# Performance work log

Hardware: AMD Instinct MI355X
Metric: run time of the kernel (lower is better)

The kernel has to match this reference:

```python
import jax, jax.numpy as jnp
import numpy as np

EMBED_DIM = 512
NUM_HEADS = 8
HEAD_DIM = EMBED_DIM // NUM_HEADS


def setup_inputs() -> dict:
    key = jax.random.key(0)
    k1, k2, k3, k4, k5, k6 = jax.random.split(key, 6)
    B, S, D = 2, 4096, EMBED_DIM
    scale = 1.0 / np.sqrt(D)
    return {
        "inputs": jax.random.normal(k1, (B, S, D), dtype=jnp.float32),
        "Wq": jax.random.normal(k2, (D, D), dtype=jnp.float32) * scale,
        "Wk": jax.random.normal(k3, (D, D), dtype=jnp.float32) * scale,
        "Wv": jax.random.normal(k4, (D, D), dtype=jnp.float32) * scale,
        "Wc": jax.random.normal(k5, (D, D), dtype=jnp.float32) * scale,
        "bc": jax.random.normal(k6, (D,), dtype=jnp.float32) * 0.01,
    }


def reference(inputs, Wq, Wk, Wv, Wc, bc):
    B, S, D = inputs.shape
    H, Hd = NUM_HEADS, HEAD_DIM

    def split_heads(x):
        # [B,S,D] -> [B,H,S,Hd]
        return x.reshape(B, S, H, Hd).transpose(0, 2, 1, 3)

    # nn.Linear applies x @ W.T
    q = split_heads(inputs @ Wq.T).astype(jnp.float32)
    k = split_heads(inputs @ Wk.T).astype(jnp.float32)
    v = split_heads(inputs @ Wv.T).astype(jnp.float32)

    scores = jnp.einsum("bhqd,bhkd->bhqk", q, k) / np.sqrt(Hd).astype(jnp.float32)
    weights = jax.nn.softmax(scores, axis=-1)
    attended = jnp.einsum("bhqk,bhkd->bhqd", weights, v).astype(inputs.dtype)
    attended = attended.transpose(0, 2, 1, 3).reshape(B, S, D)
    return attended @ Wc.T + bc
```

## Files before the change

kernel.cpp:

```cpp
#include <hip/hip_runtime.h>
#include <cstdint>
#include <cstddef>

typedef _Float16 half_t;
typedef half_t h8 __attribute__((ext_vector_type(8)));
typedef half_t h4 __attribute__((ext_vector_type(4)));
typedef float f4 __attribute__((ext_vector_type(4)));
typedef float f16v __attribute__((ext_vector_type(16)));
typedef unsigned int u32;

static constexpr int S_LEN  = 4096;
static constexpr int DMODEL = 512;
static constexpr int NH     = 8;
static constexpr int HD     = 64;
static constexpr int BATCH  = 2;
static constexpr int MTOK   = BATCH * S_LEN;

#define QSCALE 0.18033688011112043f

__device__ __forceinline__ void g2lds16(const void* g, void* l) {
    __builtin_amdgcn_global_load_lds(
        (const __attribute__((address_space(1))) u32*)(uintptr_t)g,
        (__attribute__((address_space(3))) u32*)(u32)(uintptr_t)l,
        16, 0, 0);
}

__device__ __forceinline__ f4 mfma16(h8 a, h8 b, f4 c) {
    return __builtin_amdgcn_mfma_f32_16x16x32_f16(a, b, c, 0, 0, 0);
}

__device__ __forceinline__ f16v mfma32(h8 a, h8 b, f16v c) {
    return __builtin_amdgcn_mfma_f32_32x32x16_f16(a, b, c, 0, 0, 0);
}

__device__ __forceinline__ u32 pkrtz(float a, float b) {
#if __has_builtin(__builtin_amdgcn_cvt_pkrtz)
    auto r = __builtin_amdgcn_cvt_pkrtz(a, b);
    return __builtin_bit_cast(u32, r);
#else
    union { half_t h[2]; u32 u; } x;
    x.h[0] = (half_t)a; x.h[1] = (half_t)b;
    return x.u;
#endif
}

__device__ __forceinline__ void plswap(u32 a, u32 b, u32& lo, u32& hi_, int hi) {
#if __has_builtin(__builtin_amdgcn_permlane32_swap)
    auto r = __builtin_amdgcn_permlane32_swap(a, b, false, false);
    lo = (u32)r[0]; hi_ = (u32)r[1];
#else
    u32 ta = __shfl_xor(a, 32);
    u32 tb = __shfl_xor(b, 32);
    lo  = hi ? tb : a;
    hi_ = hi ? b  : ta;
#endif
}

__global__ void cvt_all(const float* __restrict__ X,
                        const float* __restrict__ w0, const float* __restrict__ w1,
                        const float* __restrict__ w2, const float* __restrict__ w3,
                        half_t* __restrict__ Xh,
                        half_t* __restrict__ o0, half_t* __restrict__ o1,
                        half_t* __restrict__ o2, half_t* __restrict__ o3) {
    int bx = blockIdx.x;
    const float* in;
    half_t* out;
    float s = 1.0f;
    int i;
    if (bx < 2048) {
        in = X; out = Xh;
        i = (bx * 256 + threadIdx.x) * 8;
    } else {
        int y = (bx - 2048) >> 7;
        in  = (y==0) ? w0 : (y==1) ? w1 : (y==2) ? w2 : w3;
        out = (y==0) ? o0 : (y==1) ? o1 : (y==2) ? o2 : o3;
        if (y == 0) s = QSCALE;
        i = (((bx - 2048) & 127) * 256 + threadIdx.x) * 8;
    }
    const float4* p = (const float4*)(in + i);
    float4 a = p[0], b = p[1];
    h8 h;
    h[0]=(half_t)(a.x*s); h[1]=(half_t)(a.y*s); h[2]=(half_t)(a.z*s); h[3]=(half_t)(a.w*s);
    h[4]=(half_t)(b.x*s); h[5]=(half_t)(b.y*s); h[6]=(half_t)(b.z*s); h[7]=(half_t)(b.w*s);
    *(h8*)(out + i) = h;
}

__device__ __forceinline__ void gemm_core2(const half_t* __restrict__ A,
                                           const half_t* __restrict__ B,
                                           int m0, int n0, int Kdim,
                                           half_t* As, half_t* Bs,
                                           f4 (&acc)[2][4]) {
    const int tid  = threadIdx.x;
    const int lane = tid & 63;
    const int w    = tid >> 6;
    const int quad = lane >> 4;
    const int low  = lane & 15;
    const int wr   = (w >> 1) * 32;
    const int wc   = (w & 1) * 64;

    f4 zero = {0.f, 0.f, 0.f, 0.f};
    #pragma unroll
    for (int i = 0; i < 2; ++i)
        #pragma unroll
        for (int j = 0; j < 4; ++j) acc[i][j] = zero;

    auto stage = [&](int kk, int p) {
        {
            int c = tid;
            int row = c >> 2, cs = c & 3;
            int gc = cs ^ ((row >> 1) & 3);
            g2lds16(A + (size_t)(m0 + row) * Kdim + kk + gc * 8, As + p * 2048 + c * 8);
        }
        #pragma unroll
        for (int it = 0; it < 2; ++it) {
            int c = tid + 256 * it;
            int row = c >> 2, cs = c & 3;
            int gc = cs ^ ((row >> 1) & 3);
            g2lds16(B + (size_t)(n0 + row) * Kdim + kk + gc * 8, Bs + p * 4096 + c * 8);
        }
    };

    stage(0, 0);
    const int T = Kdim / 32;
    for (int t = 0; t < T; ++t) {
        __syncthreads();
        if (t + 1 < T) stage((t + 1) * 32, (t + 1) & 1);

        const half_t* Ac = As + (t & 1) * 2048;
        const half_t* Bc = Bs + (t & 1) * 4096;
        h8 af[2], bf[4];
        #pragma unroll
        for (int i = 0; i < 2; ++i) {
            int r = wr + i * 16 + low;
            af[i] = *(const h8*)(Ac + r * 32 + (quad ^ ((r >> 1) & 3)) * 8);
        }
        #pragma unroll
        for (int j = 0; j < 4; ++j) {
            int r = wc + j * 16 + low;
            bf[j] = *(const h8*)(Bc + r * 32 + (quad ^ ((r >> 1) & 3)) * 8);
        }
        #pragma unroll
        for (int i = 0; i < 2; ++i)
            #pragma unroll
            for (int j = 0; j < 4; ++j)
                acc[i][j] = mfma16(af[i], bf[j], acc[i][j]);
    }
}

__global__ __launch_bounds__(256, 4) void gemm_proj(
    const half_t* __restrict__ X,
    const half_t* __restrict__ Wq, const half_t* __restrict__ Wk, const half_t* __restrict__ Wv,
    half_t* __restrict__ Q, half_t* __restrict__ K, half_t* __restrict__ Vt) {
    __shared__ half_t As[2 * 64 * 32];
    __shared__ half_t Bs[2 * 128 * 32];
    const int z  = blockIdx.z;
    const int bx = blockIdx.x;

    const half_t *A, *B;
    int m0, n0;
    if (z < 2) {
        A = X; B = (z == 0) ? Wq : Wk;
        m0 = (bx >> 2) * 64; n0 = (bx & 3) * 128;
    } else {
        A = Wv; B = X;
        m0 = (bx & 7) * 64; n0 = (bx >> 3) * 128;
    }
    f4 acc[2][4];
    gemm_core2(A, B, m0, n0, DMODEL, As, Bs, acc);

    const int lane = threadIdx.x & 63;
    const int w    = threadIdx.x >> 6;
    const int quad = lane >> 4, low = lane & 15;
    const int wr = (w >> 1) * 32, wc = (w & 1) * 64;

    if (z < 2) {
        half_t* O = (z == 0) ? Q : K;
        #pragma unroll
        for (int i = 0; i < 2; ++i) {
            int mb = m0 + wr + i * 16 + quad * 4;
            #pragma unroll
            for (int j = 0; j < 4; ++j) {
                int n = n0 + wc + j * 16 + low;
                int h = n >> 6, d = n & 63;
                #pragma unroll
                for (int r = 0; r < 4; ++r) {
                    int m = mb + r;
                    int b = m >> 12, s = m & 4095;
                    size_t idx = (((size_t)(b * NH + h) << 12) + s) * 64 + d;
                    O[idx] = (half_t)acc[i][j][r];
                }
            }
        }
    } else {
        #pragma unroll
        for (int i = 0; i < 2; ++i) {
            int dgb = m0 + wr + i * 16 + quad * 4;
            #pragma unroll
            for (int j = 0; j < 4; ++j) {
                int tok = n0 + wc + j * 16 + low;
                int b = tok >> 12, s = tok & 4095;
                #pragma unroll
                for (int r = 0; r < 4; ++r) {
                    int dg = dgb + r;
                    size_t idx = (((size_t)(b * NH + (dg >> 6)) << 18)) + ((dg & 63) << 12) + s;
                    Vt[idx] = (half_t)acc[i][j][r];
                }
            }
        }
    }
}

__global__ __launch_bounds__(256, 4) void gemm_out(
    const half_t* __restrict__ A, const half_t* __restrict__ W,
    const float* __restrict__ bias, float* __restrict__ out) {
    __shared__ half_t As[2 * 64 * 32];
    __shared__ half_t Bs[2 * 128 * 32];
    const int bx = blockIdx.x;
    const int m0 = (bx >> 2) * 64;
    const int n0 = (bx & 3) * 128;
    f4 acc[2][4];
    gemm_core2(A, W, m0, n0, DMODEL, As, Bs, acc);

    const int lane = threadIdx.x & 63;
    const int w    = threadIdx.x >> 6;
    const int quad = lane >> 4, low = lane & 15;
    const int wr = (w >> 1) * 32, wc = (w & 1) * 64;

    #pragma unroll
    for (int i = 0; i < 2; ++i) {
        int mb = m0 + wr + i * 16 + quad * 4;
        #pragma unroll
        for (int j = 0; j < 4; ++j) {
            int n = n0 + wc + j * 16 + low;
            float bv = bias[n];
            #pragma unroll
            for (int r = 0; r < 4; ++r)
                out[(size_t)(mb + r) * DMODEL + n] = acc[i][j][r] + bv;
        }
    }
}

__global__ __launch_bounds__(256, 2) void flash_attn(
    const half_t* __restrict__ Q,
    const half_t* __restrict__ K,
    const half_t* __restrict__ V,
    half_t* __restrict__ Oa) {
    __shared__ half_t Ks[2][128 * 64];
    __shared__ half_t Vs[2][64 * 128];

    const int tid  = threadIdx.x;
    const int lane = tid & 63;
    const int w    = tid >> 6;
    const int l31  = lane & 31;
    const int hi   = lane >> 5;
    const int bh   = blockIdx.y;
    const int q0   = blockIdx.x * 128 + w * 32;

    const half_t* Qb = Q + ((size_t)bh << 18);
    const half_t* Kb = K + ((size_t)bh << 18);
    const half_t* Vb = V + ((size_t)bh << 18);

    h8 qf[4];
    #pragma unroll
    for (int ks = 0; ks < 4; ++ks)
        qf[ks] = *(const h8*)(Qb + (size_t)(q0 + l31) * 64 + ks * 16 + hi * 8);

    f16v zz;
    #pragma unroll
    for (int r = 0; r < 16; ++r) zz[r] = 0.f;

    f16v Oacc[2];
    Oacc[0] = zz; Oacc[1] = zz;
    f4 rs = {0.f, 0.f, 0.f, 0.f};

    auto stage = [&](int k0, int p) {
        #pragma unroll
        for (int it = 0; it < 4; ++it) {
            int c = tid + 256 * it;
            int key = c >> 3, cs = c & 7;
            int gc = cs ^ (key & 7);
            g2lds16(Kb + (size_t)(k0 + key) * 64 + gc * 8, &Ks[p][c * 8]);
        }
        #pragma unroll
        for (int it = 0; it < 4; ++it) {
            int c = tid + 256 * it;
            int d = c >> 4, cs = c & 15;
            int gc = cs ^ (d & 7);
            g2lds16(Vb + (size_t)d * S_LEN + k0 + gc * 8, &Vs[p][c * 8]);
        }
    };

    stage(0, 0);

    for (int c = 0; c < S_LEN / 128; ++c) {
        __syncthreads();
        if (c + 1 < S_LEN / 128) stage((c + 1) * 128, (c + 1) & 1);

        const half_t* Kc = Ks[c & 1];
        const half_t* Vc = Vs[c & 1];

        f16v sc[4];
        #pragma unroll
        for (int nt = 0; nt < 4; ++nt) {
            int key = nt * 32 + l31;
            #pragma unroll
            for (int ks = 0; ks < 4; ++ks) {
                h8 kf = *(const h8*)(Kc + key * 64 + ((ks * 2 + hi) ^ (key & 7)) * 8);
                sc[nt] = mfma32(kf, qf[ks], ks == 0 ? zz : sc[nt]);
            }
        }

        #pragma unroll
        for (int nt = 0; nt < 4; ++nt) {
            float p[16];
            #pragma unroll
            for (int r = 0; r < 16; ++r) {
                p[r] = __builtin_amdgcn_exp2f(sc[nt][r]);
                rs[r & 3] += p[r];
            }
            u32 a0 = pkrtz(p[0],  p[1]);
            u32 a1 = pkrtz(p[2],  p[3]);
            u32 a2 = pkrtz(p[4],  p[5]);
            u32 a3 = pkrtz(p[6],  p[7]);
            u32 a4 = pkrtz(p[8],  p[9]);
            u32 a5 = pkrtz(p[10], p[11]);
            u32 a6 = pkrtz(p[12], p[13]);
            u32 a7 = pkrtz(p[14], p[15]);

            union H8U { u32 u[4]; h8 v; } b0, b1;
            plswap(a0, a2, b0.u[0], b0.u[2], hi);
            plswap(a1, a3, b0.u[1], b0.u[3], hi);
            plswap(a4, a6, b1.u[0], b1.u[2], hi);
            plswap(a5, a7, b1.u[1], b1.u[3], hi);

            #pragma unroll
            for (int dt = 0; dt < 2; ++dt) {
                int d = dt * 32 + l31;
                h8 vf0 = *(const h8*)(Vc + d * 128 + ((nt * 4 + 0 + hi) ^ (d & 7)) * 8);
                h8 vf1 = *(const h8*)(Vc + d * 128 + ((nt * 4 + 2 + hi) ^ (d & 7)) * 8);
                Oacc[dt] = mfma32(vf0, b0.v, Oacc[dt]);
                Oacc[dt] = mfma32(vf1, b1.v, Oacc[dt]);
            }
        }
    }

    float lsum = (rs[0] + rs[1]) + (rs[2] + rs[3]);
    lsum += __shfl_xor(lsum, 32);
    float inv = 1.0f / lsum;

    const int b = bh >> 3, h = bh & 7;
    half_t* Ob = Oa + ((size_t)(b * S_LEN + q0 + l31)) * DMODEL + h * 64;
    #pragma unroll
    for (int dt = 0; dt < 2; ++dt)
        #pragma unroll
        for (int rg = 0; rg < 4; ++rg) {
            h4 o;
            #pragma unroll
            for (int e = 0; e < 4; ++e) o[e] = (half_t)(Oacc[dt][rg * 4 + e] * inv);
            *(h4*)(Ob + dt * 32 + rg * 8 + hi * 4) = o;
        }
}

extern "C" void kernel_launch(void* const* d_in, const int* in_sizes, int n_in,
                              void* d_out, int out_size, void* d_ws, size_t ws_size,
                              hipStream_t stream) {
    const float* X  = (const float*)d_in[0];
    const float* Wq = (const float*)d_in[1];
    const float* Wk = (const float*)d_in[2];
    const float* Wv = (const float*)d_in[3];
    const float* Wc = (const float*)d_in[4];
    const float* bc = (const float*)d_in[5];
    float* out = (float*)d_out;

    char* ws = (char*)d_ws;
    const size_t SZ_X = (size_t)MTOK * DMODEL * 2;
    const size_t SZ_W = (size_t)DMODEL * DMODEL * 2;
    half_t* Xh   = (half_t*)(ws);
    half_t* Wqh  = (half_t*)(ws + SZ_X);
    half_t* Wkh  = (half_t*)(ws + SZ_X + SZ_W);
    half_t* Wvh  = (half_t*)(ws + SZ_X + 2 * SZ_W);
    half_t* Wch  = (half_t*)(ws + SZ_X + 3 * SZ_W);
    half_t* Qh   = (half_t*)(ws + SZ_X + 4 * SZ_W);
    half_t* Kh   = (half_t*)(ws + 2 * SZ_X + 4 * SZ_W);
    half_t* Vt   = (half_t*)(ws + 3 * SZ_X + 4 * SZ_W);
    half_t* Att  = (half_t*)(ws + 4 * SZ_X + 4 * SZ_W);

    cvt_all<<<2048 + 512, 256, 0, stream>>>(X, Wq, Wk, Wv, Wc, Xh, Wqh, Wkh, Wvh, Wch);
    gemm_proj<<<dim3(512, 1, 3), 256, 0, stream>>>(Xh, Wqh, Wkh, Wvh, Qh, Kh, Vt);
    flash_attn<<<dim3(32, 16), 256, 0, stream>>>(Qh, Kh, Vt, Att);
    gemm_out<<<512, 256, 0, stream>>>(Att, Wch, bc, out);
}
```

Before: 203.8 us.

## Store MFMA fragments contiguously in LDS and double GEMM K-tile to 64

The GEMM and attention kernels now write global data into LDS already arranged in MFMA-fragment order, so each lane reads its operand with a single contiguous lane*8 offset. This replaces the XOR swizzle and per-fragment address arithmetic. The GEMM K step grows from 32 to 64, halving the number of barrier iterations, at the cost of twice the shared memory and a lower occupancy hint (4 to 3 blocks). Global loads become less contiguous per row (16-byte chunks scattered across rows), which may cost memory coalescing efficiency.

```diff
diff --git a/kernel.cpp b/kernel.cpp
--- a/kernel.cpp
+++ b/kernel.cpp
@@ -85,7 +85,7 @@
     *(h8*)(out + i) = h;
 }
 
-__device__ __forceinline__ void gemm_core2(const half_t* __restrict__ A,
+__device__ __forceinline__ void gemm_core3(const half_t* __restrict__ A,
                                            const half_t* __restrict__ B,
                                            int m0, int n0, int Kdim,
                                            half_t* As, half_t* Bs,
@@ -93,10 +93,8 @@
     const int tid  = threadIdx.x;
     const int lane = tid & 63;
     const int w    = tid >> 6;
+    const int low  = lane & 15;
     const int quad = lane >> 4;
-    const int low  = lane & 15;
-    const int wr   = (w >> 1) * 32;
-    const int wc   = (w & 1) * 64;
 
     f4 zero = {0.f, 0.f, 0.f, 0.f};
     #pragma unroll
@@ -104,55 +102,60 @@
         #pragma unroll
         for (int j = 0; j < 4; ++j) acc[i][j] = zero;
 
-    auto stage = [&](int kk, int p) {
-        {
-            int c = tid;
-            int row = c >> 2, cs = c & 3;
-            int gc = cs ^ ((row >> 1) & 3);
-            g2lds16(A + (size_t)(m0 + row) * Kdim + kk + gc * 8, As + p * 2048 + c * 8);
-        }
+    auto stage = [&](int kk0, int p) {
         #pragma unroll
         for (int it = 0; it < 2; ++it) {
             int c = tid + 256 * it;
-            int row = c >> 2, cs = c & 3;
-            int gc = cs ^ ((row >> 1) & 3);
-            g2lds16(B + (size_t)(n0 + row) * Kdim + kk + gc * 8, Bs + p * 4096 + c * 8);
+            int row = m0 + (c >> 7) * 16 + low;
+            int col = kk0 + ((c >> 6) & 1) * 32 + quad * 8;
+            g2lds16(A + (size_t)row * Kdim + col, As + p * 4096 + c * 8);
+        }
+        #pragma unroll
+        for (int it = 0; it < 4; ++it) {
+            int c = tid + 256 * it;
+            int row = n0 + (c >> 7) * 16 + low;
+            int col = kk0 + ((c >> 6) & 1) * 32 + quad * 8;
+            g2lds16(B + (size_t)row * Kdim + col, Bs + p * 8192 + c * 8);
         }
     };
 
     stage(0, 0);
-    const int T = Kdim / 32;
+    const int T = Kdim / 64;
+    const int aoff = (w >> 1) * 2048 + lane * 8;
+    const int boff = (w & 1) * 4096 + lane * 8;
     for (int t = 0; t < T; ++t) {
         __syncthreads();
-        if (t + 1 < T) stage((t + 1) * 32, (t + 1) & 1);
-
-        const half_t* Ac = As + (t & 1) * 2048;
-        const half_t* Bc = Bs + (t & 1) * 4096;
-        h8 af[2], bf[4];
-        #pragma unroll
-        for (int i = 0; i < 2; ++i) {
-            int r = wr + i * 16 + low;
-            af[i] = *(const h8*)(Ac + r * 32 + (quad ^ ((r >> 1) & 3)) * 8);
-        }
-        #pragma unroll
-        for (int j = 0; j < 4; ++j) {
-            int r = wc + j * 16 + low;
-            bf[j] = *(const h8*)(Bc + r * 32 + (quad ^ ((r >> 1) & 3)) * 8);
-        }
+        if (t + 1 < T) stage((t + 1) * 64, (t + 1) & 1);
+
+        const half_t* Al = As + (t & 1) * 4096 + aoff;
+        const half_t* Bl = Bs + (t & 1) * 8192 + boff;
+        h8 af[2][2], bf[4][2];
         #pragma unroll
         for (int i = 0; i < 2; ++i)
             #pragma unroll
-            for (int j = 0; j < 4; ++j)
-                acc[i][j] = mfma16(af[i], bf[j], acc[i][j]);
-    }
-}
-
-__global__ __launch_bounds__(256, 4) void gemm_proj(
+            for (int kk = 0; kk < 2; ++kk)
+                af[i][kk] = *(const h8*)(Al + i * 1024 + kk * 512);
+        #pragma unroll
+        for (int j = 0; j < 4; ++j)
+            #pragma unroll
+            for (int kk = 0; kk < 2; ++kk)
+                bf[j][kk] = *(const h8*)(Bl + j * 1024 + kk * 512);
+        #pragma unroll
+        for (int kk = 0; kk < 2; ++kk)
+            #pragma unroll
+            for (int i = 0; i < 2; ++i)
+                #pragma unroll
+                for (int j = 0; j < 4; ++j)
+                    acc[i][j] = mfma16(af[i][kk], bf[j][kk], acc[i][j]);
+    }
+}
+
+__global__ __launch_bounds__(256, 3) void gemm_proj(
     const half_t* __restrict__ X,
     const half_t* __restrict__ Wq, const half_t* __restrict__ Wk, const half_t* __restrict__ Wv,
     half_t* __restrict__ Q, half_t* __restrict__ K, half_t* __restrict__ Vt) {
-    __shared__ half_t As[2 * 64 * 32];
-    __shared__ half_t Bs[2 * 128 * 32];
+    __shared__ half_t As[2 * 64 * 64];
+    __shared__ half_t Bs[2 * 128 * 64];
     const int z  = blockIdx.z;
     const int bx = blockIdx.x;
 
@@ -166,7 +169,7 @@
         m0 = (bx & 7) * 64; n0 = (bx >> 3) * 128;
     }
     f4 acc[2][4];
-    gemm_core2(A, B, m0, n0, DMODEL, As, Bs, acc);
+    gemm_core3(A, B, m0, n0, DMODEL, As, Bs, acc);
 
     const int lane = threadIdx.x & 63;
     const int w    = threadIdx.x >> 6;
@@ -210,16 +213,16 @@
     }
 }
 
-__global__ __launch_bounds__(256, 4) void gemm_out(
+__global__ __launch_bounds__(256, 3) void gemm_out(
     const half_t* __restrict__ A, const half_t* __restrict__ W,
     const float* __restrict__ bias, float* __restrict__ out) {
-    __shared__ half_t As[2 * 64 * 32];
-    __shared__ half_t Bs[2 * 128 * 32];
+    __shared__ half_t As[2 * 64 * 64];
+    __shared__ half_t Bs[2 * 128 * 64];
     const int bx = blockIdx.x;
     const int m0 = (bx >> 2) * 64;
     const int n0 = (bx & 3) * 128;
     f4 acc[2][4];
-    gemm_core2(A, W, m0, n0, DMODEL, As, Bs, acc);
+    gemm_core3(A, W, m0, n0, DMODEL, As, Bs, acc);
 
     const int lane = threadIdx.x & 63;
     const int w    = threadIdx.x >> 6;
@@ -277,16 +280,16 @@
         #pragma unroll
         for (int it = 0; it < 4; ++it) {
             int c = tid + 256 * it;
-            int key = c >> 3, cs = c & 7;
-            int gc = cs ^ (key & 7);
-            g2lds16(Kb + (size_t)(k0 + key) * 64 + gc * 8, &Ks[p][c * 8]);
+            int key = k0 + (c >> 8) * 32 + l31;
+            int col = ((c >> 6) & 3) * 16 + hi * 8;
+            g2lds16(Kb + (size_t)key * 64 + col, &Ks[p][c * 8]);
         }
         #pragma unroll
         for (int it = 0; it < 4; ++it) {
             int c = tid + 256 * it;
-            int d = c >> 4, cs = c & 15;
-            int gc = cs ^ (d & 7);
-            g2lds16(Vb + (size_t)d * S_LEN + k0 + gc * 8, &Vs[p][c * 8]);
+            int d   = (c >> 9) * 32 + l31;
+            int key = k0 + ((c >> 6) & 7) * 16 + hi * 8;
+            g2lds16(Vb + (size_t)d * S_LEN + key, &Vs[p][c * 8]);
         }
     };
 
@@ -296,16 +299,15 @@
         __syncthreads();
         if (c + 1 < S_LEN / 128) stage((c + 1) * 128, (c + 1) & 1);
 
-        const half_t* Kc = Ks[c & 1];
-        const half_t* Vc = Vs[c & 1];
+        const half_t* Kl = Ks[c & 1] + lane * 8;
+        const half_t* Vl = Vs[c & 1] + lane * 8;
 
         f16v sc[4];
         #pragma unroll
         for (int nt = 0; nt < 4; ++nt) {
-            int key = nt * 32 + l31;
             #pragma unroll
             for (int ks = 0; ks < 4; ++ks) {
-                h8 kf = *(const h8*)(Kc + key * 64 + ((ks * 2 + hi) ^ (key & 7)) * 8);
+                h8 kf = *(const h8*)(Kl + nt * 2048 + ks * 512);
                 sc[nt] = mfma32(kf, qf[ks], ks == 0 ? zz : sc[nt]);
             }
         }
@@ -335,9 +337,8 @@
 
             #pragma unroll
             for (int dt = 0; dt < 2; ++dt) {
-                int d = dt * 32 + l31;
-                h8 vf0 = *(const h8*)(Vc + d * 128 + ((nt * 4 + 0 + hi) ^ (d & 7)) * 8);
-                h8 vf1 = *(const h8*)(Vc + d * 128 + ((nt * 4 + 2 + hi) ^ (d & 7)) * 8);
+                h8 vf0 = *(const h8*)(Vl + dt * 4096 + (nt * 2 + 0) * 512);
+                h8 vf1 = *(const h8*)(Vl + dt * 4096 + (nt * 2 + 1) * 512);
                 Oacc[dt] = mfma32(vf0, b0.v, Oacc[dt]);
                 Oacc[dt] = mfma32(vf1, b1.v, Oacc[dt]);
             }
```

After: 216.0 us. 6.0% more time.

## Enlarge GEMM tiles to 128x128 and pre-fragment K/V LDS layout in attention

Applied to the files above, without the earlier changes.

The projection and output GEMMs move from 64x128 to 128x128 block tiles, with each wave computing 64x64 and accumulating in a 4x4 MFMA grid. This halves the grid and raises data reuse per LDS load, at the cost of more registers and LDS per block and lower occupancy (launch bounds 3). The flash attention kernel now stages K and V into LDS already arranged in MFMA fragment order, so each lane reads contiguous 16-byte chunks at a fixed offset instead of computing XOR-swizzled addresses.

```diff
diff --git a/kernel.cpp b/kernel.cpp
--- a/kernel.cpp
+++ b/kernel.cpp
@@ -85,31 +85,32 @@
     *(h8*)(out + i) = h;
 }
 
-__device__ __forceinline__ void gemm_core2(const half_t* __restrict__ A,
+__device__ __forceinline__ void gemm_core4(const half_t* __restrict__ A,
                                            const half_t* __restrict__ B,
                                            int m0, int n0, int Kdim,
                                            half_t* As, half_t* Bs,
-                                           f4 (&acc)[2][4]) {
+                                           f4 (&acc)[4][4]) {
     const int tid  = threadIdx.x;
     const int lane = tid & 63;
     const int w    = tid >> 6;
     const int quad = lane >> 4;
     const int low  = lane & 15;
-    const int wr   = (w >> 1) * 32;
+    const int wr   = (w >> 1) * 64;
     const int wc   = (w & 1) * 64;
 
     f4 zero = {0.f, 0.f, 0.f, 0.f};
     #pragma unroll
-    for (int i = 0; i < 2; ++i)
+    for (int i = 0; i < 4; ++i)
         #pragma unroll
         for (int j = 0; j < 4; ++j) acc[i][j] = zero;
 
     auto stage = [&](int kk, int p) {
-        {
-            int c = tid;
+        #pragma unroll
+        for (int it = 0; it < 2; ++it) {
+            int c = tid + 256 * it;
             int row = c >> 2, cs = c & 3;
             int gc = cs ^ ((row >> 1) & 3);
-            g2lds16(A + (size_t)(m0 + row) * Kdim + kk + gc * 8, As + p * 2048 + c * 8);
+            g2lds16(A + (size_t)(m0 + row) * Kdim + kk + gc * 8, As + p * 4096 + c * 8);
         }
         #pragma unroll
         for (int it = 0; it < 2; ++it) {
@@ -126,11 +127,11 @@
         __syncthreads();
         if (t + 1 < T) stage((t + 1) * 32, (t + 1) & 1);
 
-        const half_t* Ac = As + (t & 1) * 2048;
+        const half_t* Ac = As + (t & 1) * 4096;
         const half_t* Bc = Bs + (t & 1) * 4096;
-        h8 af[2], bf[4];
-        #pragma unroll
-        for (int i = 0; i < 2; ++i) {
+        h8 af[4], bf[4];
+        #pragma unroll
+        for (int i = 0; i < 4; ++i) {
             int r = wr + i * 16 + low;
             af[i] = *(const h8*)(Ac + r * 32 + (quad ^ ((r >> 1) & 3)) * 8);
         }
@@ -140,18 +141,18 @@
             bf[j] = *(const h8*)(Bc + r * 32 + (quad ^ ((r >> 1) & 3)) * 8);
         }
         #pragma unroll
-        for (int i = 0; i < 2; ++i)
+        for (int i = 0; i < 4; ++i)
             #pragma unroll
             for (int j = 0; j < 4; ++j)
                 acc[i][j] = mfma16(af[i], bf[j], acc[i][j]);
     }
 }
 
-__global__ __launch_bounds__(256, 4) void gemm_proj(
+__global__ __launch_bounds__(256, 3) void gemm_proj(
     const half_t* __restrict__ X,
     const half_t* __restrict__ Wq, const half_t* __restrict__ Wk, const half_t* __restrict__ Wv,
     half_t* __restrict__ Q, half_t* __restrict__ K, half_t* __restrict__ Vt) {
-    __shared__ half_t As[2 * 64 * 32];
+    __shared__ half_t As[2 * 128 * 32];
     __shared__ half_t Bs[2 * 128 * 32];
     const int z  = blockIdx.z;
     const int bx = blockIdx.x;
@@ -160,23 +161,23 @@
     int m0, n0;
     if (z < 2) {
         A = X; B = (z == 0) ? Wq : Wk;
-        m0 = (bx >> 2) * 64; n0 = (bx & 3) * 128;
+        m0 = (bx >> 2) * 128; n0 = (bx & 3) * 128;
     } else {
         A = Wv; B = X;
-        m0 = (bx & 7) * 64; n0 = (bx >> 3) * 128;
-    }
-    f4 acc[2][4];
-    gemm_core2(A, B, m0, n0, DMODEL, As, Bs, acc);
+        m0 = (bx & 3) * 128; n0 = (bx >> 2) * 128;
+    }
+    f4 acc[4][4];
+    gemm_core4(A, B, m0, n0, DMODEL, As, Bs, acc);
 
     const int lane = threadIdx.x & 63;
     const int w    = threadIdx.x >> 6;
     const int quad = lane >> 4, low = lane & 15;
-    const int wr = (w >> 1) * 32, wc = (w & 1) * 64;
+    const int wr = (w >> 1) * 64, wc = (w & 1) * 64;
 
     if (z < 2) {
         half_t* O = (z == 0) ? Q : K;
         #pragma unroll
-        for (int i = 0; i < 2; ++i) {
+        for (int i = 0; i < 4; ++i) {
             int mb = m0 + wr + i * 16 + quad * 4;
             #pragma unroll
             for (int j = 0; j < 4; ++j) {
@@ -193,7 +194,7 @@
         }
     } else {
         #pragma unroll
-        for (int i = 0; i < 2; ++i) {
+        for (int i = 0; i < 4; ++i) {
             int dgb = m0 + wr + i * 16 + quad * 4;
             #pragma unroll
             for (int j = 0; j < 4; ++j) {
@@ -210,24 +211,24 @@
     }
 }
 
-__global__ __launch_bounds__(256, 4) void gemm_out(
+__global__ __launch_bounds__(256, 3) void gemm_out(
     const half_t* __restrict__ A, const half_t* __restrict__ W,
     const float* __restrict__ bias, float* __restrict__ out) {
-    __shared__ half_t As[2 * 64 * 32];
+    __shared__ half_t As[2 * 128 * 32];
     __shared__ half_t Bs[2 * 128 * 32];
     const int bx = blockIdx.x;
-    const int m0 = (bx >> 2) * 64;
+    const int m0 = (bx >> 2) * 128;
     const int n0 = (bx & 3) * 128;
-    f4 acc[2][4];
-    gemm_core2(A, W, m0, n0, DMODEL, As, Bs, acc);
+    f4 acc[4][4];
+    gemm_core4(A, W, m0, n0, DMODEL, As, Bs, acc);
 
     const int lane = threadIdx.x & 63;
     const int w    = threadIdx.x >> 6;
     const int quad = lane >> 4, low = lane & 15;
-    const int wr = (w >> 1) * 32, wc = (w & 1) * 64;
-
-    #pragma unroll
-    for (int i = 0; i < 2; ++i) {
+    const int wr = (w >> 1) * 64, wc = (w & 1) * 64;
+
+    #pragma unroll
+    for (int i = 0; i < 4; ++i) {
         int mb = m0 + wr + i * 16 + quad * 4;
         #pragma unroll
         for (int j = 0; j < 4; ++j) {
@@ -277,16 +278,16 @@
         #pragma unroll
         for (int it = 0; it < 4; ++it) {
             int c = tid + 256 * it;
-            int key = c >> 3, cs = c & 7;
-            int gc = cs ^ (key & 7);
-            g2lds16(Kb + (size_t)(k0 + key) * 64 + gc * 8, &Ks[p][c * 8]);
+            int key = k0 + (c >> 8) * 32 + l31;
+            int col = ((c >> 6) & 3) * 16 + hi * 8;
+            g2lds16(Kb + (size_t)key * 64 + col, &Ks[p][c * 8]);
         }
         #pragma unroll
         for (int it = 0; it < 4; ++it) {
             int c = tid + 256 * it;
-            int d = c >> 4, cs = c & 15;
-            int gc = cs ^ (d & 7);
-            g2lds16(Vb + (size_t)d * S_LEN + k0 + gc * 8, &Vs[p][c * 8]);
+            int d   = (c >> 9) * 32 + l31;
+            int key = k0 + ((c >> 6) & 7) * 16 + hi * 8;
+            g2lds16(Vb + (size_t)d * S_LEN + key, &Vs[p][c * 8]);
         }
     };
 
@@ -296,16 +297,15 @@
         __syncthreads();
         if (c + 1 < S_LEN / 128) stage((c + 1) * 128, (c + 1) & 1);
 
-        const half_t* Kc = Ks[c & 1];
-        const half_t* Vc = Vs[c & 1];
+        const half_t* Kl = Ks[c & 1] + lane * 8;
+        const half_t* Vl = Vs[c & 1] + lane * 8;
 
         f16v sc[4];
         #pragma unroll
         for (int nt = 0; nt < 4; ++nt) {
-            int key = nt * 32 + l31;
             #pragma unroll
             for (int ks = 0; ks < 4; ++ks) {
-                h8 kf = *(const h8*)(Kc + key * 64 + ((ks * 2 + hi) ^ (key & 7)) * 8);
+                h8 kf = *(const h8*)(Kl + nt * 2048 + ks * 512);
                 sc[nt] = mfma32(kf, qf[ks], ks == 0 ? zz : sc[nt]);
             }
         }
@@ -335,9 +335,8 @@
 
             #pragma unroll
             for (int dt = 0; dt < 2; ++dt) {
-                int d = dt * 32 + l31;
-                h8 vf0 = *(const h8*)(Vc + d * 128 + ((nt * 4 + 0 + hi) ^ (d & 7)) * 8);
-                h8 vf1 = *(const h8*)(Vc + d * 128 + ((nt * 4 + 2 + hi) ^ (d & 7)) * 8);
+                h8 vf0 = *(const h8*)(Vl + dt * 4096 + (nt * 2 + 0) * 512);
+                h8 vf1 = *(const h8*)(Vl + dt * 4096 + (nt * 2 + 1) * 512);
                 Oacc[dt] = mfma32(vf0, b0.v, Oacc[dt]);
                 Oacc[dt] = mfma32(vf1, b1.v, Oacc[dt]);
             }
@@ -386,7 +385,7 @@
     half_t* Att  = (half_t*)(ws + 4 * SZ_X + 4 * SZ_W);
 
     cvt_all<<<2048 + 512, 256, 0, stream>>>(X, Wq, Wk, Wv, Wc, Xh, Wqh, Wkh, Wvh, Wch);
-    gemm_proj<<<dim3(512, 1, 3), 256, 0, stream>>>(Xh, Wqh, Wkh, Wvh, Qh, Kh, Vt);
+    gemm_proj<<<dim3(256, 1, 3), 256, 0, stream>>>(Xh, Wqh, Wkh, Wvh, Qh, Kh, Vt);
     flash_attn<<<dim3(32, 16), 256, 0, stream>>>(Qh, Kh, Vt, Att);
-    gemm_out<<<512, 256, 0, stream>>>(Att, Wch, bc, out);
-}
+    gemm_out<<<256, 256, 0, stream>>>(Att, Wch, bc, out);
+}
```

New measurement: 198.9 us. 1.02x faster.
